# Performance work log

Measured on AMD Instinct MI355X. Metric: run time of the kernel, lower is better.

## Reference

```python
import jax, jax.numpy as jnp
import numpy as np

N, E, D, H, DH, M = 100000, 1600000, 128, 8, 16, 3  # nodes, edges, model_dim, heads, head_dim, views
NEG = -1e9


def setup_inputs() -> dict:
    key = jax.random.key(0)
    ks = jax.random.split(key, 12)
    x = jax.random.normal(ks[0], (N, D), jnp.float32)
    src = jax.random.randint(ks[1], (E,), 0, N)
    dst = jax.random.randint(ks[2], (E,), 0, N)
    pi = jax.random.uniform(ks[3], (N, H, M), jnp.float32)
    pi = pi / pi.sum(-1, keepdims=True)  # router mixture over views
    view_w = jax.random.uniform(ks[4], (E, M), jnp.float32)
    s = 1.0 / np.sqrt(D)
    Wq = jax.random.normal(ks[5], (D, D), jnp.float32) * s
    Wk = jax.random.normal(ks[6], (D, D), jnp.float32) * s
    Wv = jax.random.normal(ks[7], (D, D), jnp.float32) * s
    bq = jax.random.normal(ks[8], (D,), jnp.float32) * 0.02
    bk = jax.random.normal(ks[9], (D,), jnp.float32) * 0.02
    bv = jax.random.normal(ks[10], (D,), jnp.float32) * 0.02
    return {"x": x, "pi": pi, "view_w": view_w, "Wq": Wq, "bq": bq,
            "Wk": Wk, "bk": bk, "Wv": Wv, "bv": bv, "src": src, "dst": dst}


def reference(x, pi, view_w, Wq, bq, Wk, bk, Wv, bv, src, dst):
    n = x.shape[0]
    q = (x @ Wq + bq).reshape(n, H, DH)
    k = (x @ Wk + bk).reshape(n, H, DH)
    v = (x @ Wv + bv).reshape(n, H, DH)
    # per-edge mixture weight: sum over views of pi[dst] * view_w  -> [E, H]
    mix = jnp.einsum('ehm,em->eh', pi[dst], view_w)
    raw = jnp.einsum('ehd,ehd->eh', q[dst], k[src]) / jnp.sqrt(jnp.float32(DH))
    scores = raw + jnp.log(jnp.clip(mix, 1e-8))  # adjacency_mode == 'bias'
    valid = mix > 0
    masked = jnp.where(valid, scores, NEG)
    # scatter-softmax over incoming edges per (node, head)
    smax = jax.ops.segment_max(masked, dst, num_segments=n)
    expv = jnp.where(valid, jnp.exp(masked - smax[dst]), 0.0)
    ssum = jax.ops.segment_sum(expv, dst, num_segments=n)
    attn = expv / jnp.maximum(ssum[dst], 1e-8)  # [E, H]
    # weighted scatter-sum aggregation -> [N, H, DH]
    node_states = jax.ops.segment_sum(v[src] * attn[:, :, None], dst, num_segments=n)
    return node_states, attn
```

## Files before the change

kernel.cpp:

```cpp
#include <hip/hip_runtime.h>
#include <hip/hip_bf16.h>
#include <math.h>

#define SCAN_CHUNK 2048

typedef _Float16 half2v __attribute__((ext_vector_type(2)));
typedef _Float16 half8 __attribute__((ext_vector_type(8)));
typedef _Float16 half16v __attribute__((ext_vector_type(16)));
typedef float floatx4 __attribute__((ext_vector_type(4)));

#if defined(__has_builtin)
#if __has_builtin(__builtin_amdgcn_fdot2)
#define USE_FDOT2 1
#endif
#endif


__global__ void hist_kernel(const int* __restrict__ dst, int* __restrict__ counts, int e) {
    int i = blockIdx.x * blockDim.x + threadIdx.x;
    if (i < e) atomicAdd(&counts[dst[i]], 1);
}

__global__ __launch_bounds__(256) void scan_block_sums(const int* __restrict__ counts,
                                                       int* __restrict__ bsum, int n) {
    __shared__ int sd[256];
    int t = threadIdx.x;
    int base = blockIdx.x * SCAN_CHUNK + t * 8;
    int s = 0;
#pragma unroll
    for (int j = 0; j < 8; ++j) {
        int idx = base + j;
        if (idx < n) s += counts[idx];
    }
    sd[t] = s;
    __syncthreads();
    for (int off = 128; off > 0; off >>= 1) {
        if (t < off) sd[t] += sd[t + off];
        __syncthreads();
    }
    if (t == 0) bsum[blockIdx.x] = sd[0];
}

__global__ void scan_wave(int* bsum, int nb) {
    int lane = threadIdx.x;
    int orig = (lane < nb) ? bsum[lane] : 0;
    int v = orig;
    for (int off = 1; off < 64; off <<= 1) {
        int t = __shfl_up(v, off, 64);
        if (lane >= off) v += t;
    }
    if (lane < nb) bsum[lane] = v - orig;
}

__global__ __launch_bounds__(256) void scan_write(const int* __restrict__ counts,
                                                  const int* __restrict__ bsum,
                                                  int* __restrict__ row_ptr,
                                                  int* __restrict__ cursor,
                                                  int n, int total) {
    __shared__ int sd[256];
    int t = threadIdx.x;
    int base = blockIdx.x * SCAN_CHUNK + t * 8;
    int v[8];
    int s = 0;
#pragma unroll
    for (int j = 0; j < 8; ++j) {
        int idx = base + j;
        v[j] = (idx < n) ? counts[idx] : 0;
        s += v[j];
    }
    sd[t] = s;
    __syncthreads();
    for (int off = 1; off < 256; off <<= 1) {
        int tmp = 0;
        if (t >= off) tmp = sd[t - off];
        __syncthreads();
        if (t >= off) sd[t] += tmp;
        __syncthreads();
    }
    int run = bsum[blockIdx.x] + sd[t] - s;
#pragma unroll
    for (int j = 0; j < 8; ++j) {
        int idx = base + j;
        if (idx < n) {
            row_ptr[idx] = run;
            cursor[idx] = run;
            run += v[j];
        }
    }
    if (blockIdx.x == 0 && t == 0) row_ptr[n] = total;
}

__global__ void fill_csr(const int* __restrict__ dst, const int* __restrict__ src,
                         int* cursor, int2* __restrict__ csr2, int e) {
    int i = blockIdx.x * blockDim.x + threadIdx.x;
    if (i < e) {
        int p = atomicAdd(&cursor[dst[i]], 1);
        csr2[p] = make_int2(i, src[i]);
    }
}


__global__ __launch_bounds__(256) void convert_x(const float* __restrict__ x,
                                                 _Float16* __restrict__ xh, int total8) {
    int i = blockIdx.x * blockDim.x + threadIdx.x;
    if (i < total8) {
        const float4* s = (const float4*)x + i * 2;
        float4 a = s[0], b = s[1];
        half8 h;
        h[0] = (_Float16)a.x; h[1] = (_Float16)a.y; h[2] = (_Float16)a.z; h[3] = (_Float16)a.w;
        h[4] = (_Float16)b.x; h[5] = (_Float16)b.y; h[6] = (_Float16)b.z; h[7] = (_Float16)b.w;
        *((half8*)xh + i) = h;
    }
}

__global__ __launch_bounds__(256) void prep_w(const float* __restrict__ Wq,
                                              const float* __restrict__ Wk,
                                              const float* __restrict__ Wv,
                                              _Float16* __restrict__ wt) {
    const float* W = (blockIdx.x == 0) ? Wq : (blockIdx.x == 1) ? Wk : Wv;
    _Float16* out = wt + (size_t)blockIdx.x * 16384;
    int t = threadIdx.x;
    for (int r = 0; r < 64; ++r) {
        int idx = r * 256 + t;
        int k = idx >> 7, nn = idx & 127;
        out[nn * 128 + k] = (_Float16)W[idx];
    }
}


#define LDP 136

__global__ __launch_bounds__(256) void qkv_mfma(
    const _Float16* __restrict__ xh, const _Float16* __restrict__ wt,
    const float* __restrict__ bq, const float* __restrict__ bk,
    const float* __restrict__ bv,
    _Float16* __restrict__ qh, _Float16* __restrict__ kh, _Float16* __restrict__ vh,
    int n) {
    __shared__ __align__(16) _Float16 xs[128 * LDP];
    __shared__ __align__(16) _Float16 ws[128 * LDP];

    int t = threadIdx.x;
    int tile0 = blockIdx.x * 128;
    int sel = blockIdx.y;
    const _Float16* wsel = wt + (size_t)sel * 16384;
    const float* bias = (sel == 0) ? bq : (sel == 1) ? bk : bv;
    _Float16* out = (sel == 0) ? qh : (sel == 1) ? kh : vh;

#pragma unroll
    for (int r = 0; r < 8; ++r) {
        int id = r * 256 + t;
        int row = id >> 4, c8 = id & 15;
        int grow = tile0 + row;
        half8 val = (half8)(_Float16)0;
        if (grow < n) val = *((const half8*)(xh + (size_t)grow * 128) + c8);
        *((half8*)(xs + row * LDP) + c8) = val;
        half8 wv = *((const half8*)(wsel + row * 128) + c8);
        *((half8*)(ws + row * LDP) + c8) = wv;
    }
    __syncthreads();

    int wave = t >> 6, lane = t & 63;
    int wm = (wave & 1) * 64, wn = (wave >> 1) * 64;
    int lrow = lane & 15, quad = lane >> 4;

    floatx4 acc[4][4];
#pragma unroll
    for (int i = 0; i < 4; ++i)
#pragma unroll
        for (int j = 0; j < 4; ++j) acc[i][j] = (floatx4)0.f;

#pragma unroll
    for (int kk = 0; kk < 4; ++kk) {
        int kbase = kk * 32 + quad * 8;
        half8 a[4], b[4];
#pragma unroll
        for (int i = 0; i < 4; ++i)
            a[i] = *(const half8*)(xs + (wm + i * 16 + lrow) * LDP + kbase);
#pragma unroll
        for (int j = 0; j < 4; ++j)
            b[j] = *(const half8*)(ws + (wn + j * 16 + lrow) * LDP + kbase);
#pragma unroll
        for (int i = 0; i < 4; ++i)
#pragma unroll
            for (int j = 0; j < 4; ++j)
                acc[i][j] = __builtin_amdgcn_mfma_f32_16x16x32_f16(a[i], b[j], acc[i][j], 0, 0, 0);
    }

#pragma unroll
    for (int i = 0; i < 4; ++i) {
#pragma unroll
        for (int j = 0; j < 4; ++j) {
            int col = wn + j * 16 + lrow;
            float bv_ = bias[col];
#pragma unroll
            for (int r = 0; r < 4; ++r) {
                int row = wm + i * 16 + quad * 4 + r;
                int grow = tile0 + row;
                if (grow < n) out[(size_t)grow * 128 + col] = (_Float16)(acc[i][j][r] + bv_);
            }
        }
    }
}


#define PREFETCH(S, idx)                                                      \
    {                                                                         \
        k##S = (half16v)(_Float16)0; v##S = (half16v)(_Float16)0;             \
        w##S##0 = 0.f; w##S##1 = 0.f; w##S##2 = 0.f;                          \
        if ((idx) < end) {                                                    \
            k##S = *(const half16v*)(kbase + (size_t)m##S.y * 128);           \
            v##S = *(const half16v*)(vbase + (size_t)m##S.y * 128);           \
            const float* vp_ = view_w + (size_t)m##S.x * 3;                   \
            w##S##0 = vp_[0]; w##S##1 = vp_[1]; w##S##2 = vp_[2];             \
        }                                                                     \
    }

#ifdef USE_FDOT2
#define DOT16(dres, kS)                                                       \
    {                                                                         \
        _Pragma("unroll")                                                     \
        for (int j_ = 0; j_ < 8; ++j_) {                                      \
            half2v a_, b_;                                                    \
            a_[0] = qv[2 * j_]; a_[1] = qv[2 * j_ + 1];                       \
            b_[0] = kS[2 * j_]; b_[1] = kS[2 * j_ + 1];                       \
            dres = __builtin_amdgcn_fdot2(a_, b_, dres, false);               \
        }                                                                     \
    }
#else
#define DOT16(dres, kS)                                                       \
    {                                                                         \
        _Pragma("unroll")                                                     \
        for (int j_ = 0; j_ < 16; ++j_)                                       \
            dres = fmaf((float)qv[j_], (float)kS[j_], dres);                  \
    }
#endif

#define COMPUTE(S, eidx, valid)                                               \
    {                                                                         \
        float mix_ = fmaf(p0, w##S##0, fmaf(p1, w##S##1, p2 * w##S##2));      \
        float d_ = 0.f;                                                       \
        DOT16(d_, k##S);                                                      \
        float p_ = (mix_ > 0.f) ? mix_ * __expf(d_ * 0.25f) : 0.f;            \
        if (valid) pbuf[(size_t)(eidx)*8 + h] = (_Float16)p_;                 \
        l += p_;                                                              \
        _Pragma("unroll")                                                     \
        for (int j_ = 0; j_ < 16; ++j_)                                       \
            acc[j_] = fmaf(p_, (float)v##S[j_], acc[j_]);                     \
    }

#define BODY(S0, S1, S2, S3, jj)                                              \
    {                                                                         \
        PREFETCH(S2, (jj) + 2);                                               \
        PREFETCH(S3, (jj) + 3);                                               \
        int eA_ = m##S0.x, eB_ = m##S1.x;                                     \
        m##S0 = make_int2(0, 0); m##S1 = make_int2(0, 0);                     \
        if ((jj) + 4 < end) m##S0 = csr2[(jj) + 4];                           \
        if ((jj) + 5 < end) m##S1 = csr2[(jj) + 5];                           \
        COMPUTE(S0, eA_, true);                                               \
        COMPUTE(S1, eB_, (jj) + 1 < end);                                     \
    }

__global__ __launch_bounds__(256) void edge_attn(
    const _Float16* __restrict__ qh, const _Float16* __restrict__ kh,
    const _Float16* __restrict__ vh, const float* __restrict__ pi,
    const float* __restrict__ view_w,
    const int* __restrict__ row_ptr, const int2* __restrict__ csr2,
    float* __restrict__ node_out, float* __restrict__ invb,
    _Float16* __restrict__ pbuf, int n) {
    int t = threadIdx.x;
    int node = blockIdx.x * 32 + (t >> 3);
    if (node >= n) return;
    int h = t & 7;

    const half16v qv = *(const half16v*)(qh + (size_t)node * 128 + h * 16);
    const _Float16* kbase = kh + h * 16;
    const _Float16* vbase = vh + h * 16;

    float p0 = pi[node * 24 + h * 3 + 0];
    float p1 = pi[node * 24 + h * 3 + 1];
    float p2 = pi[node * 24 + h * 3 + 2];
    int beg = row_ptr[node], end = row_ptr[node + 1];

    float l = 0.f;
    float acc[16];
#pragma unroll
    for (int j = 0; j < 16; ++j) acc[j] = 0.f;

    int2 mA = make_int2(0, 0), mB = make_int2(0, 0);
    int2 mC = make_int2(0, 0), mD = make_int2(0, 0);
    float wA0 = 0.f, wA1 = 0.f, wA2 = 0.f, wB0 = 0.f, wB1 = 0.f, wB2 = 0.f;
    float wC0 = 0.f, wC1 = 0.f, wC2 = 0.f, wD0 = 0.f, wD1 = 0.f, wD2 = 0.f;
    half16v kA = (half16v)(_Float16)0, vA = kA, kB = kA, vB = kA;
    half16v kC = kA, vC = kA, kD = kA, vD = kA;

    if (beg < end)     mA = csr2[beg];
    if (beg + 1 < end) mB = csr2[beg + 1];
    if (beg + 2 < end) mC = csr2[beg + 2];
    if (beg + 3 < end) mD = csr2[beg + 3];
    PREFETCH(A, beg);
    PREFETCH(B, beg + 1);

    for (int j = beg; j < end;) {
        BODY(A, B, C, D, j);
        j += 2;
        if (j >= end) break;
        BODY(C, D, A, B, j);
        j += 2;
    }

    float inv = 1.f / fmaxf(l, 1e-8f);
    invb[(size_t)node * 8 + h] = inv;

    float4* op = (float4*)(node_out + (size_t)node * 128 + h * 16);
#pragma unroll
    for (int j = 0; j < 4; ++j)
        op[j] = make_float4(acc[4 * j] * inv, acc[4 * j + 1] * inv,
                            acc[4 * j + 2] * inv, acc[4 * j + 3] * inv);
}


__global__ __launch_bounds__(256) void attn_norm(
    const _Float16* __restrict__ pbuf, const int* __restrict__ dst,
    const float* __restrict__ invb, float* __restrict__ attn_out, int e) {
    int i = blockIdx.x * blockDim.x + threadIdx.x;
    if (i < e) {
        int d = dst[i];
        half8 p = *((const half8*)pbuf + i);
        const float4* iv = (const float4*)(invb + (size_t)d * 8);
        float4 i0 = iv[0], i1 = iv[1];
        float4* op = (float4*)(attn_out + (size_t)i * 8);
        op[0] = make_float4((float)p[0] * i0.x, (float)p[1] * i0.y,
                            (float)p[2] * i0.z, (float)p[3] * i0.w);
        op[1] = make_float4((float)p[4] * i1.x, (float)p[5] * i1.y,
                            (float)p[6] * i1.z, (float)p[7] * i1.w);
    }
}


extern "C" void kernel_launch(void* const* d_in, const int* in_sizes, int n_in,
                              void* d_out, int out_size, void* d_ws, size_t ws_size,
                              hipStream_t stream) {
    const float* x  = (const float*)d_in[0];
    const float* pi = (const float*)d_in[1];
    const float* vw = (const float*)d_in[2];
    const float* Wq = (const float*)d_in[3];
    const float* bq = (const float*)d_in[4];
    const float* Wk = (const float*)d_in[5];
    const float* bk = (const float*)d_in[6];
    const float* Wv = (const float*)d_in[7];
    const float* bv = (const float*)d_in[8];
    const int* src  = (const int*)d_in[9];
    const int* dst  = (const int*)d_in[10];

    int n = in_sizes[0] / 128;
    int e = in_sizes[9];

    _Float16* xh = (_Float16*)d_ws;
    _Float16* qh = xh + (size_t)n * 128;
    _Float16* kh = qh + (size_t)n * 128;
    _Float16* vh = kh + (size_t)n * 128;
    _Float16* wt = vh + (size_t)n * 128;
    _Float16* pbuf = wt + 3 * 16384;
    float* invb  = (float*)(pbuf + (size_t)e * 8);
    int* counts  = (int*)(invb + (size_t)n * 8);
    int* cursor  = counts + n;
    int* row_ptr = cursor + n;
    int* bsum    = row_ptr + n + 1;

    float* node_out = (float*)d_out;
    float* attn_out = node_out + (size_t)n * 128;
    int2* csr2 = (int2*)attn_out;

    hipMemsetAsync(counts, 0, (size_t)n * sizeof(int), stream);

    int eb = (e + 255) / 256;
    hist_kernel<<<eb, 256, 0, stream>>>(dst, counts, e);

    int nb = (n + SCAN_CHUNK - 1) / SCAN_CHUNK;
    scan_block_sums<<<nb, 256, 0, stream>>>(counts, bsum, n);
    scan_wave<<<1, 64, 0, stream>>>(bsum, nb);
    scan_write<<<nb, 256, 0, stream>>>(counts, bsum, row_ptr, cursor, n, e);
    fill_csr<<<eb, 256, 0, stream>>>(dst, src, cursor, csr2, e);

    int tot8 = (n * 128) / 8;
    convert_x<<<(tot8 + 255) / 256, 256, 0, stream>>>(x, xh, tot8);
    prep_w<<<3, 256, 0, stream>>>(Wq, Wk, Wv, wt);

    int gtiles = (n + 127) / 128;
    qkv_mfma<<<dim3(gtiles, 3), 256, 0, stream>>>(xh, wt, bq, bk, bv, qh, kh, vh, n);

    int gb = (n + 31) / 32;
    edge_attn<<<gb, 256, 0, stream>>>(qh, kh, vh, pi, vw, row_ptr, csr2,
                                      node_out, invb, pbuf, n);
    attn_norm<<<eb, 256, 0, stream>>>(pbuf, dst, invb, attn_out, e);
}
```

Measured before the change: 646.3 us.

## Pack view weights into CSR records and split each head across two lanes

fill_csr now writes a 16-byte record per edge (src, edge id, view weights as fp16), so the edge loop no longer gathers view_w by edge index. edge_attn assigns two lanes per (node, head), each handling 8 of the 16 head dims and combining the dot product with a shuffle. Blocks shrink to 64 threads covering 4 nodes with a launch-bounds occupancy hint. This cuts per-thread registers and the scattered view_w loads, at the cost of a wider CSR record, an extra shuffle per edge, and fp16 rounding of the view weights.

Result: faster. 619.3 us (-4.2%).

```diff
diff --git a/kernel.cpp b/kernel.cpp
--- a/kernel.cpp
+++ b/kernel.cpp
@@ -6,7 +6,6 @@
 
 typedef _Float16 half2v __attribute__((ext_vector_type(2)));
 typedef _Float16 half8 __attribute__((ext_vector_type(8)));
-typedef _Float16 half16v __attribute__((ext_vector_type(16)));
 typedef float floatx4 __attribute__((ext_vector_type(4)));
 
 #if defined(__has_builtin)
@@ -91,11 +90,21 @@
 }
 
 __global__ void fill_csr(const int* __restrict__ dst, const int* __restrict__ src,
-                         int* cursor, int2* __restrict__ csr2, int e) {
+                         const float* __restrict__ vw, int* cursor,
+                         int4* __restrict__ recs, int e) {
     int i = blockIdx.x * blockDim.x + threadIdx.x;
     if (i < e) {
         int p = atomicAdd(&cursor[dst[i]], 1);
-        csr2[p] = make_int2(i, src[i]);
+        float w0 = vw[3 * i], w1 = vw[3 * i + 1], w2 = vw[3 * i + 2];
+        unsigned u0 = (unsigned)__builtin_bit_cast(unsigned short, (_Float16)w0);
+        unsigned u1 = (unsigned)__builtin_bit_cast(unsigned short, (_Float16)w1);
+        unsigned u2 = (unsigned)__builtin_bit_cast(unsigned short, (_Float16)w2);
+        int4 r;
+        r.x = src[i];
+        r.y = i;
+        r.z = (int)(u0 | (u1 << 16));
+        r.w = (int)u2;
+        recs[p] = r;
     }
 }
 
@@ -203,78 +212,95 @@
 }
 
 
-#define PREFETCH(S, idx)                                                      \
-    {                                                                         \
-        k##S = (half16v)(_Float16)0; v##S = (half16v)(_Float16)0;             \
-        w##S##0 = 0.f; w##S##1 = 0.f; w##S##2 = 0.f;                          \
+#define STAGE_META(S, idx)                                                    \
+    {                                                                         \
+        s##S = 0; e##S = 0; m##S = 0.f;                                       \
         if ((idx) < end) {                                                    \
-            k##S = *(const half16v*)(kbase + (size_t)m##S.y * 128);           \
-            v##S = *(const half16v*)(vbase + (size_t)m##S.y * 128);           \
-            const float* vp_ = view_w + (size_t)m##S.x * 3;                   \
-            w##S##0 = vp_[0]; w##S##1 = vp_[1]; w##S##2 = vp_[2];             \
+            int4 r_ = recs[(idx)];                                            \
+            s##S = r_.x; e##S = r_.y;                                         \
+            half2v w01_ = __builtin_bit_cast(half2v, r_.z);                   \
+            _Float16 w2_ =                                                    \
+                __builtin_bit_cast(_Float16, (unsigned short)(unsigned)r_.w); \
+            m##S = fmaf(p0, (float)w01_[0],                                   \
+                        fmaf(p1, (float)w01_[1], p2 * (float)w2_));           \
         }                                                                     \
     }
 
+#define ISSUE_KV(S, idx)                                                      \
+    {                                                                         \
+        k##S = (half8)(_Float16)0; v##S = (half8)(_Float16)0;                 \
+        if ((idx) < end) {                                                    \
+            k##S = *(const half8*)(kbase + (size_t)s##S * 128);               \
+            v##S = *(const half8*)(vbase + (size_t)s##S * 128);               \
+        }                                                                     \
+    }
+
 #ifdef USE_FDOT2
-#define DOT16(dres, kS)                                                       \
+#define DOT8(dres, kS)                                                        \
     {                                                                         \
         _Pragma("unroll")                                                     \
-        for (int j_ = 0; j_ < 8; ++j_) {                                      \
-            half2v a_, b_;                                                    \
-            a_[0] = qv[2 * j_]; a_[1] = qv[2 * j_ + 1];                       \
-            b_[0] = kS[2 * j_]; b_[1] = kS[2 * j_ + 1];                       \
-            dres = __builtin_amdgcn_fdot2(a_, b_, dres, false);               \
+        for (int jj_ = 0; jj_ < 4; ++jj_) {                                   \
+            half2v x_, y_;                                                    \
+            x_[0] = qv[2 * jj_]; x_[1] = qv[2 * jj_ + 1];                     \
+            y_[0] = kS[2 * jj_]; y_[1] = kS[2 * jj_ + 1];                     \
+            dres = __builtin_amdgcn_fdot2(x_, y_, dres, false);               \
         }                                                                     \
     }
 #else
-#define DOT16(dres, kS)                                                       \
+#define DOT8(dres, kS)                                                        \
     {                                                                         \
         _Pragma("unroll")                                                     \
-        for (int j_ = 0; j_ < 16; ++j_)                                       \
-            dres = fmaf((float)qv[j_], (float)kS[j_], dres);                  \
+        for (int jj_ = 0; jj_ < 8; ++jj_)                                     \
+            dres = fmaf((float)qv[jj_], (float)kS[jj_], dres);                \
     }
 #endif
 
-#define COMPUTE(S, eidx, valid)                                               \
-    {                                                                         \
-        float mix_ = fmaf(p0, w##S##0, fmaf(p1, w##S##1, p2 * w##S##2));      \
+#define COMPUTE(S, mx, ev, validc)                                            \
+    {                                                                         \
         float d_ = 0.f;                                                       \
-        DOT16(d_, k##S);                                                      \
-        float p_ = (mix_ > 0.f) ? mix_ * __expf(d_ * 0.25f) : 0.f;            \
-        if (valid) pbuf[(size_t)(eidx)*8 + h] = (_Float16)p_;                 \
+        DOT8(d_, k##S);                                                       \
+        d_ += __shfl_xor(d_, 1, 64);                                          \
+        float p_ = ((mx) > 0.f) ? (mx)*__expf(d_ * 0.25f) : 0.f;              \
+        if (sub == 0 && (validc)) pbuf[(size_t)(ev)*8 + h] = (_Float16)p_;    \
         l += p_;                                                              \
-        _Pragma("unroll")                                                     \
-        for (int j_ = 0; j_ < 16; ++j_)                                       \
-            acc[j_] = fmaf(p_, (float)v##S[j_], acc[j_]);                     \
+        a0 = fmaf(p_, (float)v##S[0], a0);                                    \
+        a1 = fmaf(p_, (float)v##S[1], a1);                                    \
+        a2 = fmaf(p_, (float)v##S[2], a2);                                    \
+        a3 = fmaf(p_, (float)v##S[3], a3);                                    \
+        a4 = fmaf(p_, (float)v##S[4], a4);                                    \
+        a5 = fmaf(p_, (float)v##S[5], a5);                                    \
+        a6 = fmaf(p_, (float)v##S[6], a6);                                    \
+        a7 = fmaf(p_, (float)v##S[7], a7);                                    \
     }
 
 #define BODY(S0, S1, S2, S3, jj)                                              \
     {                                                                         \
-        PREFETCH(S2, (jj) + 2);                                               \
-        PREFETCH(S3, (jj) + 3);                                               \
-        int eA_ = m##S0.x, eB_ = m##S1.x;                                     \
-        m##S0 = make_int2(0, 0); m##S1 = make_int2(0, 0);                     \
-        if ((jj) + 4 < end) m##S0 = csr2[(jj) + 4];                           \
-        if ((jj) + 5 < end) m##S1 = csr2[(jj) + 5];                           \
-        COMPUTE(S0, eA_, true);                                               \
-        COMPUTE(S1, eB_, (jj) + 1 < end);                                     \
-    }
-
-__global__ __launch_bounds__(256) void edge_attn(
+        ISSUE_KV(S2, (jj) + 2);                                               \
+        ISSUE_KV(S3, (jj) + 3);                                               \
+        float mx0_ = m##S0, mx1_ = m##S1;                                     \
+        int ev0_ = e##S0, ev1_ = e##S1;                                       \
+        STAGE_META(S0, (jj) + 4);                                             \
+        STAGE_META(S1, (jj) + 5);                                             \
+        COMPUTE(S0, mx0_, ev0_, true);                                        \
+        COMPUTE(S1, mx1_, ev1_, (jj) + 1 < end);                              \
+    }
+
+__global__ __launch_bounds__(64, 6) void edge_attn(
     const _Float16* __restrict__ qh, const _Float16* __restrict__ kh,
     const _Float16* __restrict__ vh, const float* __restrict__ pi,
-    const float* __restrict__ view_w,
-    const int* __restrict__ row_ptr, const int2* __restrict__ csr2,
+    const int* __restrict__ row_ptr, const int4* __restrict__ recs,
     float* __restrict__ node_out, float* __restrict__ invb,
     _Float16* __restrict__ pbuf, int n) {
     int t = threadIdx.x;
-    int node = blockIdx.x * 32 + (t >> 3);
+    int node = blockIdx.x * 4 + (t >> 4);
     if (node >= n) return;
-    int h = t & 7;
-
-    const half16v qv = *(const half16v*)(qh + (size_t)node * 128 + h * 16);
-    const _Float16* kbase = kh + h * 16;
-    const _Float16* vbase = vh + h * 16;
+    int q16 = t & 15;
+    int h = q16 >> 1, sub = q16 & 1;
+    int off = h * 16 + sub * 8;
+
+    const half8 qv = *(const half8*)(qh + (size_t)node * 128 + off);
+    const _Float16* kbase = kh + off;
+    const _Float16* vbase = vh + off;
 
     float p0 = pi[node * 24 + h * 3 + 0];
     float p1 = pi[node * 24 + h * 3 + 1];
@@ -282,23 +308,19 @@
     int beg = row_ptr[node], end = row_ptr[node + 1];
 
     float l = 0.f;
-    float acc[16];
-#pragma unroll
-    for (int j = 0; j < 16; ++j) acc[j] = 0.f;
-
-    int2 mA = make_int2(0, 0), mB = make_int2(0, 0);
-    int2 mC = make_int2(0, 0), mD = make_int2(0, 0);
-    float wA0 = 0.f, wA1 = 0.f, wA2 = 0.f, wB0 = 0.f, wB1 = 0.f, wB2 = 0.f;
-    float wC0 = 0.f, wC1 = 0.f, wC2 = 0.f, wD0 = 0.f, wD1 = 0.f, wD2 = 0.f;
-    half16v kA = (half16v)(_Float16)0, vA = kA, kB = kA, vB = kA;
-    half16v kC = kA, vC = kA, kD = kA, vD = kA;
-
-    if (beg < end)     mA = csr2[beg];
-    if (beg + 1 < end) mB = csr2[beg + 1];
-    if (beg + 2 < end) mC = csr2[beg + 2];
-    if (beg + 3 < end) mD = csr2[beg + 3];
-    PREFETCH(A, beg);
-    PREFETCH(B, beg + 1);
+    float a0 = 0.f, a1 = 0.f, a2 = 0.f, a3 = 0.f;
+    float a4 = 0.f, a5 = 0.f, a6 = 0.f, a7 = 0.f;
+
+    int sA, eA, sB, eB, sC, eC, sD, eD;
+    float mA, mB, mC, mD;
+    half8 kA, vA, kB, vB, kC, vC, kD, vD;
+
+    STAGE_META(A, beg);
+    STAGE_META(B, beg + 1);
+    STAGE_META(C, beg + 2);
+    STAGE_META(D, beg + 3);
+    ISSUE_KV(A, beg);
+    ISSUE_KV(B, beg + 1);
 
     for (int j = beg; j < end;) {
         BODY(A, B, C, D, j);
@@ -309,13 +331,11 @@
     }
 
     float inv = 1.f / fmaxf(l, 1e-8f);
-    invb[(size_t)node * 8 + h] = inv;
-
-    float4* op = (float4*)(node_out + (size_t)node * 128 + h * 16);
-#pragma unroll
-    for (int j = 0; j < 4; ++j)
-        op[j] = make_float4(acc[4 * j] * inv, acc[4 * j + 1] * inv,
-                            acc[4 * j + 2] * inv, acc[4 * j + 3] * inv);
+    if (sub == 0) invb[(size_t)node * 8 + h] = inv;
+
+    float4* op = (float4*)(node_out + (size_t)node * 128 + off);
+    op[0] = make_float4(a0 * inv, a1 * inv, a2 * inv, a3 * inv);
+    op[1] = make_float4(a4 * inv, a5 * inv, a6 * inv, a7 * inv);
 }
 
 
@@ -369,7 +389,7 @@
 
     float* node_out = (float*)d_out;
     float* attn_out = node_out + (size_t)n * 128;
-    int2* csr2 = (int2*)attn_out;
+    int4* recs = (int4*)attn_out;
 
     hipMemsetAsync(counts, 0, (size_t)n * sizeof(int), stream);
 
@@ -380,7 +400,7 @@
     scan_block_sums<<<nb, 256, 0, stream>>>(counts, bsum, n);
     scan_wave<<<1, 64, 0, stream>>>(bsum, nb);
     scan_write<<<nb, 256, 0, stream>>>(counts, bsum, row_ptr, cursor, n, e);
-    fill_csr<<<eb, 256, 0, stream>>>(dst, src, cursor, csr2, e);
+    fill_csr<<<eb, 256, 0, stream>>>(dst, src, vw, cursor, recs, e);
 
     int tot8 = (n * 128) / 8;
     convert_x<<<(tot8 + 255) / 256, 256, 0, stream>>>(x, xh, tot8);
@@ -389,8 +409,8 @@
     int gtiles = (n + 127) / 128;
     qkv_mfma<<<dim3(gtiles, 3), 256, 0, stream>>>(xh, wt, bq, bk, bv, qh, kh, vh, n);
 
-    int gb = (n + 31) / 32;
-    edge_attn<<<gb, 256, 0, stream>>>(qh, kh, vh, pi, vw, row_ptr, csr2,
-                                      node_out, invb, pbuf, n);
+    int gb = (n + 3) / 4;
+    edge_attn<<<gb, 64, 0, stream>>>(qh, kh, vh, pi, row_ptr, recs,
+                                     node_out, invb, pbuf, n);
     attn_norm<<<eb, 256, 0, stream>>>(pbuf, dst, invb, attn_out, e);
 }
```
